# Performance work log

Measured on AMD Instinct MI355X. Metric: run time of the kernel, lower is better.

Reference implementation:

```python
import jax, jax.numpy as jnp
import numpy as np

N = 50000      # nodes
E = 800000     # directed edges
D = 128        # input_dim == hidden_dim
EL = 100000    # edges scored by decoder


def setup_inputs() -> dict:
    key = jax.random.key(0)
    ks = jax.random.split(key, 8)
    s = 1.0 / np.sqrt(D)  # glorot-ish scale
    return {
        "node_feature": jax.random.normal(ks[0], (N, D), jnp.float32),
        "W1": jax.random.normal(ks[1], (D, D), jnp.float32) * s,
        "b1": jnp.zeros((D,), jnp.float32),
        "W2": jax.random.normal(ks[2], (D, D), jnp.float32) * s,
        "b2": jnp.zeros((D,), jnp.float32),
        "W3": jax.random.normal(ks[3], (D, D), jnp.float32) * s,
        "b3": jnp.zeros((D,), jnp.float32),
        "edge_index": jax.random.randint(ks[4], (2, E), 0, N, dtype=jnp.int32),
        "edge_label_index": jax.random.randint(ks[5], (2, EL), 0, N, dtype=jnp.int32),
    }


def _gcn_conv(x, W, b, src, dst, norm, n):
    # x' = D^{-1/2} (A + I) D^{-1/2} (x W) + b   (PyG GCNConv semantics)
    h = x @ W                                   # [N, D]
    msg = h[src] * norm[:, None]                # gather + scale, [E+N, D]
    out = jax.ops.segment_sum(msg, dst, num_segments=n)  # scatter-add
    return out + b


def reference(node_feature, W1, b1, W2, b2, W3, b3, edge_index, edge_label_index):
    n = node_feature.shape[0]
    loop = jnp.arange(n, dtype=edge_index.dtype)
    src = jnp.concatenate([edge_index[0], loop])  # self-loops appended
    dst = jnp.concatenate([edge_index[1], loop])
    # symmetric normalization: deg over destinations (incl. self-loops)
    deg = jax.ops.segment_sum(jnp.ones_like(dst, dtype=node_feature.dtype), dst, num_segments=n)
    dinv = jax.lax.rsqrt(jnp.maximum(deg, 1.0))
    norm = dinv[src] * dinv[dst]                 # [E+N]

    x = jax.nn.relu(_gcn_conv(node_feature, W1, b1, src, dst, norm, n))
    x = jax.nn.relu(_gcn_conv(x, W2, b2, src, dst, norm, n))
    x = _gcn_conv(x, W3, b3, src, dst, norm, n)

    # dot-product edge decoder
    u = x[edge_label_index[0]]
    v = x[edge_label_index[1]]
    return jnp.sum(u * v, axis=-1)               # [EL] logits
```

## Files before the change

### kernel.cpp

```cpp
#include <hip/hip_runtime.h>
#include <hip/hip_bf16.h>
#include <hip/hip_fp16.h>

typedef _Float16 v8h __attribute__((ext_vector_type(8)));
typedef _Float16 v4h __attribute__((ext_vector_type(4)));
typedef float v4f __attribute__((ext_vector_type(4)));

__global__ __launch_bounds__(256) void wswz(const float* __restrict__ W1,
                                            const float* __restrict__ W2,
                                            const float* __restrict__ W3,
                                            __half* __restrict__ wfrag) {
    int o = blockIdx.x * 256 + threadIdx.x;
    int w = o >> 14, r = o & 16383;
    const float* Ws = (w >= 3) ? W3 : ((w == 2) ? W2 : W1);
    float v = Ws[r];
    __half h;
    if (w == 1) {
        __half hv = __float2half_rn(v);
        h = __float2half_rn(v - __half2float(hv));
    } else {
        h = __float2half_rn(v);
    }
    int k = r >> 7, ncol = r & 127;
    int c = ncol >> 4, nl = ncol & 15;
    int s = k >> 5, quad = (k >> 3) & 3, j = k & 7;
    int di = ((c * 4 + s) * 64 + quad * 16 + nl) * 8 + j;
    wfrag[(size_t)w * 16384 + di] = h;
}

__global__ __launch_bounds__(256) void deg_rank(const int* __restrict__ dst,
                                                int* __restrict__ cnt,
                                                int* __restrict__ rank, int E) {
    int base = blockIdx.x * 1024 + threadIdx.x * 4;
    if (base + 3 < E) {
        int4 d = *(const int4*)&dst[base];
        int r0 = atomicAdd(&cnt[d.x], 1);
        int r1 = atomicAdd(&cnt[d.y], 1);
        int r2 = atomicAdd(&cnt[d.z], 1);
        int r3 = atomicAdd(&cnt[d.w], 1);
        *(int4*)&rank[base] = make_int4(r0, r1, r2, r3);
    } else {
        for (int e = base; e < E; ++e) rank[e] = atomicAdd(&cnt[dst[e]], 1);
    }
}

__global__ __launch_bounds__(256) void gemm1(const float* __restrict__ X,
                                             const __half* __restrict__ wfrag,
                                             __half* __restrict__ H, int Nrows) {
    int tid = threadIdx.x;
    int rowbase = blockIdx.x * 64;
    int l = tid & 63;
    int wid = tid >> 6;
    int rb = wid * 16;
    int quad = l >> 4;
    int nn = l & 15;
    int gr = rowbase + rb + nn;
    v8h ah[4], al[4];
    if (gr < Nrows) {
        const float* Xr = &X[(size_t)gr * 128 + quad * 8];
#pragma unroll
        for (int k = 0; k < 4; ++k) {
            float4 f0 = *(const float4*)&Xr[k * 32];
            float4 f1 = *(const float4*)&Xr[k * 32 + 4];
            float ff[8] = {f0.x, f0.y, f0.z, f0.w, f1.x, f1.y, f1.z, f1.w};
            v8h h, lo;
#pragma unroll
            for (int m = 0; m < 8; ++m) {
                _Float16 hv = (_Float16)ff[m];
                h[m] = hv;
                lo[m] = (_Float16)(ff[m] - (float)hv);
            }
            ah[k] = h;
            al[k] = lo;
        }
    } else {
#pragma unroll
        for (int k = 0; k < 4; ++k) {
            v8h z;
#pragma unroll
            for (int m = 0; m < 8; ++m) z[m] = (_Float16)0.f;
            ah[k] = z;
            al[k] = z;
        }
    }
    const v8h* Wh = (const v8h*)wfrag;
    const v8h* Wl = (const v8h*)(wfrag + 16384);
    v4f acc[8] = {};
    v8h bh0 = Wh[0 * 64 + l];
    v8h bh1 = Wh[1 * 64 + l];
    v8h bh2 = Wh[2 * 64 + l];
    v8h bh3 = Wh[3 * 64 + l];
#pragma unroll
    for (int c = 0; c < 8; ++c) {
        v8h bl0 = Wl[(c * 4 + 0) * 64 + l];
        v8h bl1 = Wl[(c * 4 + 1) * 64 + l];
        v8h bl2 = Wl[(c * 4 + 2) * 64 + l];
        v8h bl3 = Wl[(c * 4 + 3) * 64 + l];
        acc[c] = __builtin_amdgcn_mfma_f32_16x16x32_f16(ah[0], bh0, acc[c], 0, 0, 0);
        acc[c] = __builtin_amdgcn_mfma_f32_16x16x32_f16(ah[1], bh1, acc[c], 0, 0, 0);
        acc[c] = __builtin_amdgcn_mfma_f32_16x16x32_f16(ah[2], bh2, acc[c], 0, 0, 0);
        acc[c] = __builtin_amdgcn_mfma_f32_16x16x32_f16(ah[3], bh3, acc[c], 0, 0, 0);
        acc[c] = __builtin_amdgcn_mfma_f32_16x16x32_f16(al[0], bh0, acc[c], 0, 0, 0);
        acc[c] = __builtin_amdgcn_mfma_f32_16x16x32_f16(al[1], bh1, acc[c], 0, 0, 0);
        acc[c] = __builtin_amdgcn_mfma_f32_16x16x32_f16(al[2], bh2, acc[c], 0, 0, 0);
        acc[c] = __builtin_amdgcn_mfma_f32_16x16x32_f16(al[3], bh3, acc[c], 0, 0, 0);
        v8h nh0, nh1, nh2, nh3;
        if (c < 7) {
            nh0 = Wh[((c + 1) * 4 + 0) * 64 + l];
            nh1 = Wh[((c + 1) * 4 + 1) * 64 + l];
            nh2 = Wh[((c + 1) * 4 + 2) * 64 + l];
            nh3 = Wh[((c + 1) * 4 + 3) * 64 + l];
        }
        acc[c] = __builtin_amdgcn_mfma_f32_16x16x32_f16(ah[0], bl0, acc[c], 0, 0, 0);
        acc[c] = __builtin_amdgcn_mfma_f32_16x16x32_f16(ah[1], bl1, acc[c], 0, 0, 0);
        acc[c] = __builtin_amdgcn_mfma_f32_16x16x32_f16(ah[2], bl2, acc[c], 0, 0, 0);
        acc[c] = __builtin_amdgcn_mfma_f32_16x16x32_f16(ah[3], bl3, acc[c], 0, 0, 0);
        if (c < 7) { bh0 = nh0; bh1 = nh1; bh2 = nh2; bh3 = nh3; }
    }
#pragma unroll
    for (int reg = 0; reg < 4; ++reg) {
        int grr = rowbase + rb + quad * 4 + reg;
        if (grr < Nrows) {
#pragma unroll
            for (int c = 0; c < 8; ++c)
                H[(size_t)grr * 128 + c * 16 + nn] = __float2half_rn(acc[c][reg]);
        }
    }
}

__global__ __launch_bounds__(256) void agg_gemm(const __half* __restrict__ Xs,
                                                const float* __restrict__ dinv,
                                                const int* __restrict__ rowptr,
                                                const int* __restrict__ col,
                                                const __half* __restrict__ wfrag,
                                                const float* __restrict__ bias,
                                                __half* __restrict__ Out,
                                                int n, int finalLayer) {
    __shared__ __align__(16) _Float16 y[64][136];
    int tid = threadIdx.x;
    int rowbase = blockIdx.x * 64;
    {
        int sub = tid >> 4;
        int t = (tid & 15) * 8;
        for (int g = 0; g < 4; ++g) {
            int rr = g * 16 + sub;
            int node = rowbase + rr;
            float a[8] = {};
            if (node < n) {
                int beg = rowptr[node], end = rowptr[node + 1];
                int k = beg;
                for (; k + 8 <= end; k += 8) {
                    int s0 = col[k], s1 = col[k + 1], s2 = col[k + 2], s3 = col[k + 3];
                    int s4 = col[k + 4], s5 = col[k + 5], s6 = col[k + 6], s7 = col[k + 7];
                    uint4 r0 = *(const uint4*)&Xs[(size_t)s0 * 128 + t];
                    uint4 r1 = *(const uint4*)&Xs[(size_t)s1 * 128 + t];
                    uint4 r2 = *(const uint4*)&Xs[(size_t)s2 * 128 + t];
                    uint4 r3 = *(const uint4*)&Xs[(size_t)s3 * 128 + t];
                    uint4 r4 = *(const uint4*)&Xs[(size_t)s4 * 128 + t];
                    uint4 r5 = *(const uint4*)&Xs[(size_t)s5 * 128 + t];
                    uint4 r6 = *(const uint4*)&Xs[(size_t)s6 * 128 + t];
                    uint4 r7 = *(const uint4*)&Xs[(size_t)s7 * 128 + t];
                    const __half2* h0 = (const __half2*)&r0;
                    const __half2* h1 = (const __half2*)&r1;
                    const __half2* h2 = (const __half2*)&r2;
                    const __half2* h3 = (const __half2*)&r3;
                    const __half2* h4 = (const __half2*)&r4;
                    const __half2* h5 = (const __half2*)&r5;
                    const __half2* h6 = (const __half2*)&r6;
                    const __half2* h7 = (const __half2*)&r7;
#pragma unroll
                    for (int m = 0; m < 4; ++m) {
                        float2 f0 = __half22float2(h0[m]);
                        float2 f1 = __half22float2(h1[m]);
                        float2 f2 = __half22float2(h2[m]);
                        float2 f3 = __half22float2(h3[m]);
                        float2 f4 = __half22float2(h4[m]);
                        float2 f5 = __half22float2(h5[m]);
                        float2 f6 = __half22float2(h6[m]);
                        float2 f7 = __half22float2(h7[m]);
                        a[2 * m]     += ((f0.x + f1.x) + (f2.x + f3.x)) + ((f4.x + f5.x) + (f6.x + f7.x));
                        a[2 * m + 1] += ((f0.y + f1.y) + (f2.y + f3.y)) + ((f4.y + f5.y) + (f6.y + f7.y));
                    }
                }
                for (; k + 4 <= end; k += 4) {
                    int s0 = col[k], s1 = col[k + 1], s2 = col[k + 2], s3 = col[k + 3];
                    uint4 r0 = *(const uint4*)&Xs[(size_t)s0 * 128 + t];
                    uint4 r1 = *(const uint4*)&Xs[(size_t)s1 * 128 + t];
                    uint4 r2 = *(const uint4*)&Xs[(size_t)s2 * 128 + t];
                    uint4 r3 = *(const uint4*)&Xs[(size_t)s3 * 128 + t];
                    const __half2* h0 = (const __half2*)&r0;
                    const __half2* h1 = (const __half2*)&r1;
                    const __half2* h2 = (const __half2*)&r2;
                    const __half2* h3 = (const __half2*)&r3;
#pragma unroll
                    for (int m = 0; m < 4; ++m) {
                        float2 f0 = __half22float2(h0[m]);
                        float2 f1 = __half22float2(h1[m]);
                        float2 f2 = __half22float2(h2[m]);
                        float2 f3 = __half22float2(h3[m]);
                        a[2 * m]     += (f0.x + f1.x) + (f2.x + f3.x);
                        a[2 * m + 1] += (f0.y + f1.y) + (f2.y + f3.y);
                    }
                }
                for (; k < end; ++k) {
                    uint4 r0 = *(const uint4*)&Xs[(size_t)col[k] * 128 + t];
                    const __half2* h0 = (const __half2*)&r0;
#pragma unroll
                    for (int m = 0; m < 4; ++m) {
                        float2 f0 = __half22float2(h0[m]);
                        a[2 * m] += f0.x;
                        a[2 * m + 1] += f0.y;
                    }
                }
                float dn = dinv[node];
#pragma unroll
                for (int m = 0; m < 8; ++m) a[m] *= dn;
            }
            v8h yv;
#pragma unroll
            for (int m = 0; m < 8; ++m) yv[m] = (_Float16)a[m];
            *(v8h*)&y[rr][t] = yv;
        }
    }
    __syncthreads();
    int l = tid & 63;
    int wid = tid >> 6;
    int rb = wid * 16;
    int quad = l >> 4;
    int nn = l & 15;
    v8h a0 = *(const v8h*)&y[rb + nn][0 * 32 + quad * 8];
    v8h a1 = *(const v8h*)&y[rb + nn][1 * 32 + quad * 8];
    v8h a2 = *(const v8h*)&y[rb + nn][2 * 32 + quad * 8];
    v8h a3 = *(const v8h*)&y[rb + nn][3 * 32 + quad * 8];
    const v8h* Wf = (const v8h*)wfrag;
    v4f acc[8] = {};
#pragma unroll
    for (int c = 0; c < 8; ++c) {
        v8h b0 = Wf[(c * 4 + 0) * 64 + l];
        v8h b1 = Wf[(c * 4 + 1) * 64 + l];
        v8h b2 = Wf[(c * 4 + 2) * 64 + l];
        v8h b3 = Wf[(c * 4 + 3) * 64 + l];
        acc[c] = __builtin_amdgcn_mfma_f32_16x16x32_f16(a0, b0, acc[c], 0, 0, 0);
        acc[c] = __builtin_amdgcn_mfma_f32_16x16x32_f16(a1, b1, acc[c], 0, 0, 0);
        acc[c] = __builtin_amdgcn_mfma_f32_16x16x32_f16(a2, b2, acc[c], 0, 0, 0);
        acc[c] = __builtin_amdgcn_mfma_f32_16x16x32_f16(a3, b3, acc[c], 0, 0, 0);
    }
#pragma unroll
    for (int reg = 0; reg < 4; ++reg) {
        int gr = rowbase + rb + quad * 4 + reg;
        if (gr < n) {
            float dn = dinv[gr];
#pragma unroll
            for (int c = 0; c < 8; ++c) {
                float z = acc[c][reg] + bias[c * 16 + nn];
                if (!finalLayer) z = fmaxf(z, 0.f) * dn;
                Out[(size_t)gr * 128 + c * 16 + nn] = __float2half_rn(z);
            }
        }
    }
}

__global__ void scanA(const int* __restrict__ cnt, int* __restrict__ tmp,
                      int* __restrict__ bsum, int n) {
    __shared__ int s[256];
    int i = blockIdx.x * 256 + threadIdx.x;
    int v = (i < n) ? (cnt[i] + 1) : 0;
    s[threadIdx.x] = v;
    __syncthreads();
    for (int off = 1; off < 256; off <<= 1) {
        int x = (threadIdx.x >= off) ? s[threadIdx.x - off] : 0;
        __syncthreads();
        s[threadIdx.x] += x;
        __syncthreads();
    }
    if (i < n) tmp[i] = s[threadIdx.x];
    if (threadIdx.x == 255) bsum[blockIdx.x] = s[255];
}

__global__ void scanB(const int* __restrict__ tmp, const int* __restrict__ bsum,
                      const int* __restrict__ cnt, int* __restrict__ rowptr,
                      float* __restrict__ dinv, int* __restrict__ col, int n, int nb) {
    __shared__ int p[256];
    int t = threadIdx.x;
    p[t] = (t < nb) ? bsum[t] : 0;
    __syncthreads();
    for (int off = 1; off < 256; off <<= 1) {
        int x = (t >= off) ? p[t - off] : 0;
        __syncthreads();
        p[t] += x;
        __syncthreads();
    }
    int prefix = (blockIdx.x == 0) ? 0 : p[blockIdx.x - 1];
    int i = blockIdx.x * 256 + t;
    if (i < n) {
        int inc = tmp[i] + prefix;
        rowptr[i + 1] = inc;
        int c1 = cnt[i] + 1;
        dinv[i] = rsqrtf((float)c1);
        col[inc - c1] = i;
        if (i == 0) rowptr[0] = 0;
    }
}

__global__ __launch_bounds__(256) void fill4(const int* __restrict__ src,
                                             const int* __restrict__ dst,
                                             const int* __restrict__ rank,
                                             const int* __restrict__ rowptr,
                                             int* __restrict__ col, int E) {
    int base = blockIdx.x * 1024 + threadIdx.x * 4;
    if (base + 3 < E) {
        int d0 = dst[base], d1 = dst[base + 1], d2 = dst[base + 2], d3 = dst[base + 3];
        int s0 = src[base], s1 = src[base + 1], s2 = src[base + 2], s3 = src[base + 3];
        int r0 = rank[base], r1 = rank[base + 1], r2 = rank[base + 2], r3 = rank[base + 3];
        col[rowptr[d0] + 1 + r0] = s0;
        col[rowptr[d1] + 1 + r1] = s1;
        col[rowptr[d2] + 1 + r2] = s2;
        col[rowptr[d3] + 1 + r3] = s3;
    } else {
        for (int e = base; e < E; ++e)
            col[rowptr[dst[e]] + 1 + rank[e]] = src[e];
    }
}

__global__ __launch_bounds__(256) void agg_h(const __half* __restrict__ H,
                                             const float* __restrict__ dinv,
                                             const int* __restrict__ rowptr,
                                             const int* __restrict__ col,
                                             const float* __restrict__ bias,
                                             __half* __restrict__ out, int n) {
    int node = blockIdx.x * 16 + (threadIdx.x >> 4);
    int t = (threadIdx.x & 15) * 8;
    if (node >= n) return;
    int beg = rowptr[node], end = rowptr[node + 1];
    float a[8] = {};
    int k = beg;
    for (; k + 8 <= end; k += 8) {
        int s0 = col[k], s1 = col[k + 1], s2 = col[k + 2], s3 = col[k + 3];
        int s4 = col[k + 4], s5 = col[k + 5], s6 = col[k + 6], s7 = col[k + 7];
        float w0 = dinv[s0], w1 = dinv[s1], w2 = dinv[s2], w3 = dinv[s3];
        float w4 = dinv[s4], w5 = dinv[s5], w6 = dinv[s6], w7 = dinv[s7];
        uint4 r0 = *(const uint4*)&H[(size_t)s0 * 128 + t];
        uint4 r1 = *(const uint4*)&H[(size_t)s1 * 128 + t];
        uint4 r2 = *(const uint4*)&H[(size_t)s2 * 128 + t];
        uint4 r3 = *(const uint4*)&H[(size_t)s3 * 128 + t];
        uint4 r4 = *(const uint4*)&H[(size_t)s4 * 128 + t];
        uint4 r5 = *(const uint4*)&H[(size_t)s5 * 128 + t];
        uint4 r6 = *(const uint4*)&H[(size_t)s6 * 128 + t];
        uint4 r7 = *(const uint4*)&H[(size_t)s7 * 128 + t];
        const __half2* h0 = (const __half2*)&r0;
        const __half2* h1 = (const __half2*)&r1;
        const __half2* h2 = (const __half2*)&r2;
        const __half2* h3 = (const __half2*)&r3;
        const __half2* h4 = (const __half2*)&r4;
        const __half2* h5 = (const __half2*)&r5;
        const __half2* h6 = (const __half2*)&r6;
        const __half2* h7 = (const __half2*)&r7;
#pragma unroll
        for (int m = 0; m < 4; ++m) {
            float2 f0 = __half22float2(h0[m]);
            float2 f1 = __half22float2(h1[m]);
            float2 f2 = __half22float2(h2[m]);
            float2 f3 = __half22float2(h3[m]);
            float2 f4 = __half22float2(h4[m]);
            float2 f5 = __half22float2(h5[m]);
            float2 f6 = __half22float2(h6[m]);
            float2 f7 = __half22float2(h7[m]);
            a[2 * m]     += (f0.x * w0 + f1.x * w1 + f2.x * w2 + f3.x * w3)
                          + (f4.x * w4 + f5.x * w5 + f6.x * w6 + f7.x * w7);
            a[2 * m + 1] += (f0.y * w0 + f1.y * w1 + f2.y * w2 + f3.y * w3)
                          + (f4.y * w4 + f5.y * w5 + f6.y * w6 + f7.y * w7);
        }
    }
    for (; k + 4 <= end; k += 4) {
        int s0 = col[k], s1 = col[k + 1], s2 = col[k + 2], s3 = col[k + 3];
        float w0 = dinv[s0], w1 = dinv[s1], w2 = dinv[s2], w3 = dinv[s3];
        uint4 r0 = *(const uint4*)&H[(size_t)s0 * 128 + t];
        uint4 r1 = *(const uint4*)&H[(size_t)s1 * 128 + t];
        uint4 r2 = *(const uint4*)&H[(size_t)s2 * 128 + t];
        uint4 r3 = *(const uint4*)&H[(size_t)s3 * 128 + t];
        const __half2* h0 = (const __half2*)&r0;
        const __half2* h1 = (const __half2*)&r1;
        const __half2* h2 = (const __half2*)&r2;
        const __half2* h3 = (const __half2*)&r3;
#pragma unroll
        for (int m = 0; m < 4; ++m) {
            float2 f0 = __half22float2(h0[m]);
            float2 f1 = __half22float2(h1[m]);
            float2 f2 = __half22float2(h2[m]);
            float2 f3 = __half22float2(h3[m]);
            a[2 * m]     += f0.x * w0 + f1.x * w1 + f2.x * w2 + f3.x * w3;
            a[2 * m + 1] += f0.y * w0 + f1.y * w1 + f2.y * w2 + f3.y * w3;
        }
    }
    for (; k < end; ++k) {
        int s0 = col[k];
        float w0 = dinv[s0];
        uint4 r0 = *(const uint4*)&H[(size_t)s0 * 128 + t];
        const __half2* h0 = (const __half2*)&r0;
#pragma unroll
        for (int m = 0; m < 4; ++m) {
            float2 f0 = __half22float2(h0[m]);
            a[2 * m] += f0.x * w0;
            a[2 * m + 1] += f0.y * w0;
        }
    }
    float dn = dinv[node];
    float4 b0 = *(const float4*)&bias[t];
    float4 b1 = *(const float4*)&bias[t + 4];
    float r0 = fmaxf(a[0] * dn + b0.x, 0.f) * dn;
    float r1 = fmaxf(a[1] * dn + b0.y, 0.f) * dn;
    float r2 = fmaxf(a[2] * dn + b0.z, 0.f) * dn;
    float r3 = fmaxf(a[3] * dn + b0.w, 0.f) * dn;
    float r4 = fmaxf(a[4] * dn + b1.x, 0.f) * dn;
    float r5 = fmaxf(a[5] * dn + b1.y, 0.f) * dn;
    float r6 = fmaxf(a[6] * dn + b1.z, 0.f) * dn;
    float r7 = fmaxf(a[7] * dn + b1.w, 0.f) * dn;
    auto pk = [](float x, float y) { __half2 h = __floats2half2_rn(x, y); return *(unsigned int*)&h; };
    uint4 o = make_uint4(pk(r0, r1), pk(r2, r3), pk(r4, r5), pk(r6, r7));
    *(uint4*)&out[(size_t)node * 128 + t] = o;
}

__global__ __launch_bounds__(256) void decoder_h(const __half* __restrict__ X,
                                                 const int* __restrict__ eli,
                                                 float* __restrict__ out, int EL) {
    int e = blockIdx.x * 16 + (threadIdx.x >> 4);
    int lane = threadIdx.x & 15;
    if (e >= EL) return;
    int u = eli[e], v = eli[EL + e];
    uint4 ra = *(const uint4*)&X[(size_t)u * 128 + lane * 8];
    uint4 rb = *(const uint4*)&X[(size_t)v * 128 + lane * 8];
    const __half2* ha = (const __half2*)&ra;
    const __half2* hb = (const __half2*)&rb;
    float d = 0.f;
#pragma unroll
    for (int j = 0; j < 4; ++j) {
        float2 fa = __half22float2(ha[j]);
        float2 fb = __half22float2(hb[j]);
        d += fa.x * fb.x + fa.y * fb.y;
    }
#pragma unroll
    for (int off = 8; off > 0; off >>= 1) d += __shfl_xor(d, off);
    if (lane == 0) out[e] = d;
}

extern "C" void kernel_launch(void* const* d_in, const int* in_sizes, int n_in,
                              void* d_out, int out_size, void* d_ws, size_t ws_size,
                              hipStream_t stream) {
    const float* x0 = (const float*)d_in[0];
    const float* W1 = (const float*)d_in[1];
    const float* b1 = (const float*)d_in[2];
    const float* W2 = (const float*)d_in[3];
    const float* b2 = (const float*)d_in[4];
    const float* W3 = (const float*)d_in[5];
    const float* b3 = (const float*)d_in[6];
    const int* ei   = (const int*)d_in[7];
    const int* eli  = (const int*)d_in[8];
    float* out = (float*)d_out;

    const int D = 128;
    const int N  = in_sizes[0] / D;
    const int E  = in_sizes[7] / 2;
    const int EL = in_sizes[8] / 2;

    const int* src = ei;
    const int* dst = ei + E;

    char* ws = (char*)d_ws;
    size_t off = 0;
    auto alloc = [&](size_t bytes) -> void* {
        off = (off + 255) & ~(size_t)255;
        void* p = ws + off;
        off += bytes;
        return p;
    };
    int*    cnt    = (int*)alloc((size_t)N * sizeof(int));
    int*    tmp    = (int*)alloc((size_t)N * sizeof(int));
    int*    bsum   = (int*)alloc(256 * sizeof(int));
    int*    rowptr = (int*)alloc((size_t)(N + 1) * sizeof(int));
    float*  dinv   = (float*)alloc((size_t)N * sizeof(float));
    int*    rank   = (int*)alloc((size_t)E * sizeof(int));
    int*    col    = (int*)alloc((size_t)(E + N) * sizeof(int));
    __half* wfrag  = (__half*)alloc((size_t)4 * 16384 * sizeof(__half));
    __half* hbuf   = (__half*)alloc((size_t)N * D * sizeof(__half));
    __half* xbuf   = (__half*)alloc((size_t)N * D * sizeof(__half));
    (void)ws_size;

    hipMemsetAsync(cnt, 0, (size_t)N * sizeof(int), stream);

    int nbN = (N + 255) / 256;
    int nbE4 = (E + 1023) / 1024;
    int gemmGrid = (N + 63) / 64;
    int fusedGrid = (N + 63) / 64;
    int aggGrid  = (N + 15) / 16;

    wswz<<<256, 256, 0, stream>>>(W1, W2, W3, wfrag);

    deg_rank<<<nbE4, 256, 0, stream>>>(dst, cnt, rank, E);
    gemm1<<<gemmGrid, 256, 0, stream>>>(x0, wfrag, hbuf, N);

    scanA<<<nbN, 256, 0, stream>>>(cnt, tmp, bsum, N);
    scanB<<<nbN, 256, 0, stream>>>(tmp, bsum, cnt, rowptr, dinv, col, N, nbN);
    fill4<<<nbE4, 256, 0, stream>>>(src, dst, rank, rowptr, col, E);

    agg_h<<<aggGrid, 256, 0, stream>>>(hbuf, dinv, rowptr, col, b1, xbuf, N);
    agg_gemm<<<fusedGrid, 256, 0, stream>>>(xbuf, dinv, rowptr, col, wfrag + 2 * 16384, b2, hbuf, N, 0);
    agg_gemm<<<fusedGrid, 256, 0, stream>>>(hbuf, dinv, rowptr, col, wfrag + 3 * 16384, b3, xbuf, N, 1);

    decoder_h<<<(EL + 15) / 16, 256, 0, stream>>>(xbuf, eli, out, EL);
}
```

Before: 275.1 us.

## Split fused aggregation+GEMM into separate kernels and merge degree counting into gemm1

The fused agg_gemm kernel is split into agg_plain, which gathers per node with 16 nodes per 256-thread block and writes an fp16 intermediate buffer, and gemm_post, which runs the MFMA GEMM directly from global memory. The intent is better load balance and occupancy for the irregular gather, since it no longer shares a block with LDS staging and a barrier. The cost is an extra N×128 fp16 write and read per layer and two more launches. Separately, the degree/rank atomics are folded into the first GEMM launch as extra blocks, each handling 8 edges per thread, which removes one launch and lets that work run alongside the GEMM.

Result: no change. 278.2 us (+1.1%).

```diff
diff --git a/kernel.cpp b/kernel.cpp
--- a/kernel.cpp
+++ b/kernel.cpp
@@ -28,27 +28,35 @@
     wfrag[(size_t)w * 16384 + di] = h;
 }
 
-__global__ __launch_bounds__(256) void deg_rank(const int* __restrict__ dst,
-                                                int* __restrict__ cnt,
-                                                int* __restrict__ rank, int E) {
-    int base = blockIdx.x * 1024 + threadIdx.x * 4;
-    if (base + 3 < E) {
-        int4 d = *(const int4*)&dst[base];
-        int r0 = atomicAdd(&cnt[d.x], 1);
-        int r1 = atomicAdd(&cnt[d.y], 1);
-        int r2 = atomicAdd(&cnt[d.z], 1);
-        int r3 = atomicAdd(&cnt[d.w], 1);
-        *(int4*)&rank[base] = make_int4(r0, r1, r2, r3);
-    } else {
-        for (int e = base; e < E; ++e) rank[e] = atomicAdd(&cnt[dst[e]], 1);
-    }
-}
-
-__global__ __launch_bounds__(256) void gemm1(const float* __restrict__ X,
-                                             const __half* __restrict__ wfrag,
-                                             __half* __restrict__ H, int Nrows) {
+__global__ __launch_bounds__(256) void gemm1_deg(const float* __restrict__ X,
+                                                 const __half* __restrict__ wfrag,
+                                                 __half* __restrict__ H, int Nrows,
+                                                 int degBlocks,
+                                                 const int* __restrict__ dst,
+                                                 int* __restrict__ cnt,
+                                                 int* __restrict__ rank, int E) {
     int tid = threadIdx.x;
-    int rowbase = blockIdx.x * 64;
+    if (blockIdx.x < degBlocks) {
+        int base = blockIdx.x * 2048 + tid * 8;
+        if (base + 7 < E) {
+            int4 d0 = *(const int4*)&dst[base];
+            int4 d1 = *(const int4*)&dst[base + 4];
+            int r0 = atomicAdd(&cnt[d0.x], 1);
+            int r1 = atomicAdd(&cnt[d0.y], 1);
+            int r2 = atomicAdd(&cnt[d0.z], 1);
+            int r3 = atomicAdd(&cnt[d0.w], 1);
+            int r4 = atomicAdd(&cnt[d1.x], 1);
+            int r5 = atomicAdd(&cnt[d1.y], 1);
+            int r6 = atomicAdd(&cnt[d1.z], 1);
+            int r7 = atomicAdd(&cnt[d1.w], 1);
+            *(int4*)&rank[base]     = make_int4(r0, r1, r2, r3);
+            *(int4*)&rank[base + 4] = make_int4(r4, r5, r6, r7);
+        } else {
+            for (int e = base; e < E; ++e) rank[e] = atomicAdd(&cnt[dst[e]], 1);
+        }
+        return;
+    }
+    int rowbase = (blockIdx.x - degBlocks) * 64;
     int l = tid & 63;
     int wid = tid >> 6;
     int rb = wid * 16;
@@ -128,110 +136,114 @@
     }
 }
 
-__global__ __launch_bounds__(256) void agg_gemm(const __half* __restrict__ Xs,
-                                                const float* __restrict__ dinv,
-                                                const int* __restrict__ rowptr,
-                                                const int* __restrict__ col,
-                                                const __half* __restrict__ wfrag,
-                                                const float* __restrict__ bias,
-                                                __half* __restrict__ Out,
-                                                int n, int finalLayer) {
-    __shared__ __align__(16) _Float16 y[64][136];
+__global__ __launch_bounds__(256) void agg_plain(const __half* __restrict__ Xs,
+                                                 const float* __restrict__ dinv,
+                                                 const int* __restrict__ rowptr,
+                                                 const int* __restrict__ col,
+                                                 __half* __restrict__ Y, int n) {
+    int node = blockIdx.x * 16 + (threadIdx.x >> 4);
+    int t = (threadIdx.x & 15) * 8;
+    if (node >= n) return;
+    int beg = rowptr[node], end = rowptr[node + 1];
+    float a[8] = {};
+    int k = beg;
+    for (; k + 8 <= end; k += 8) {
+        int s0 = col[k], s1 = col[k + 1], s2 = col[k + 2], s3 = col[k + 3];
+        int s4 = col[k + 4], s5 = col[k + 5], s6 = col[k + 6], s7 = col[k + 7];
+        uint4 r0 = *(const uint4*)&Xs[(size_t)s0 * 128 + t];
+        uint4 r1 = *(const uint4*)&Xs[(size_t)s1 * 128 + t];
+        uint4 r2 = *(const uint4*)&Xs[(size_t)s2 * 128 + t];
+        uint4 r3 = *(const uint4*)&Xs[(size_t)s3 * 128 + t];
+        uint4 r4 = *(const uint4*)&Xs[(size_t)s4 * 128 + t];
+        uint4 r5 = *(const uint4*)&Xs[(size_t)s5 * 128 + t];
+        uint4 r6 = *(const uint4*)&Xs[(size_t)s6 * 128 + t];
+        uint4 r7 = *(const uint4*)&Xs[(size_t)s7 * 128 + t];
+        const __half2* h0 = (const __half2*)&r0;
+        const __half2* h1 = (const __half2*)&r1;
+        const __half2* h2 = (const __half2*)&r2;
+        const __half2* h3 = (const __half2*)&r3;
+        const __half2* h4 = (const __half2*)&r4;
+        const __half2* h5 = (const __half2*)&r5;
+        const __half2* h6 = (const __half2*)&r6;
+        const __half2* h7 = (const __half2*)&r7;
+#pragma unroll
+        for (int m = 0; m < 4; ++m) {
+            float2 f0 = __half22float2(h0[m]);
+            float2 f1 = __half22float2(h1[m]);
+            float2 f2 = __half22float2(h2[m]);
+            float2 f3 = __half22float2(h3[m]);
+            float2 f4 = __half22float2(h4[m]);
+            float2 f5 = __half22float2(h5[m]);
+            float2 f6 = __half22float2(h6[m]);
+            float2 f7 = __half22float2(h7[m]);
+            a[2 * m]     += ((f0.x + f1.x) + (f2.x + f3.x)) + ((f4.x + f5.x) + (f6.x + f7.x));
+            a[2 * m + 1] += ((f0.y + f1.y) + (f2.y + f3.y)) + ((f4.y + f5.y) + (f6.y + f7.y));
+        }
+    }
+    for (; k + 4 <= end; k += 4) {
+        int s0 = col[k], s1 = col[k + 1], s2 = col[k + 2], s3 = col[k + 3];
+        uint4 r0 = *(const uint4*)&Xs[(size_t)s0 * 128 + t];
+        uint4 r1 = *(const uint4*)&Xs[(size_t)s1 * 128 + t];
+        uint4 r2 = *(const uint4*)&Xs[(size_t)s2 * 128 + t];
+        uint4 r3 = *(const uint4*)&Xs[(size_t)s3 * 128 + t];
+        const __half2* h0 = (const __half2*)&r0;
+        const __half2* h1 = (const __half2*)&r1;
+        const __half2* h2 = (const __half2*)&r2;
+        const __half2* h3 = (const __half2*)&r3;
+#pragma unroll
+        for (int m = 0; m < 4; ++m) {
+            float2 f0 = __half22float2(h0[m]);
+            float2 f1 = __half22float2(h1[m]);
+            float2 f2 = __half22float2(h2[m]);
+            float2 f3 = __half22float2(h3[m]);
+            a[2 * m]     += (f0.x + f1.x) + (f2.x + f3.x);
+            a[2 * m + 1] += (f0.y + f1.y) + (f2.y + f3.y);
+        }
+    }
+    for (; k < end; ++k) {
+        uint4 r0 = *(const uint4*)&Xs[(size_t)col[k] * 128 + t];
+        const __half2* h0 = (const __half2*)&r0;
+#pragma unroll
+        for (int m = 0; m < 4; ++m) {
+            float2 f0 = __half22float2(h0[m]);
+            a[2 * m] += f0.x;
+            a[2 * m + 1] += f0.y;
+        }
+    }
+    float dn = dinv[node];
+    auto pk = [](float x, float y) { __half2 h = __floats2half2_rn(x, y); return *(unsigned int*)&h; };
+    uint4 o = make_uint4(pk(a[0] * dn, a[1] * dn), pk(a[2] * dn, a[3] * dn),
+                         pk(a[4] * dn, a[5] * dn), pk(a[6] * dn, a[7] * dn));
+    *(uint4*)&Y[(size_t)node * 128 + t] = o;
+}
+
+__global__ __launch_bounds__(256) void gemm_post(const __half* __restrict__ Y,
+                                                 const float* __restrict__ dinv,
+                                                 const __half* __restrict__ wfrag,
+                                                 const float* __restrict__ bias,
+                                                 __half* __restrict__ Out,
+                                                 int n, int finalLayer) {
     int tid = threadIdx.x;
     int rowbase = blockIdx.x * 64;
-    {
-        int sub = tid >> 4;
-        int t = (tid & 15) * 8;
-        for (int g = 0; g < 4; ++g) {
-            int rr = g * 16 + sub;
-            int node = rowbase + rr;
-            float a[8] = {};
-            if (node < n) {
-                int beg = rowptr[node], end = rowptr[node + 1];
-                int k = beg;
-                for (; k + 8 <= end; k += 8) {
-                    int s0 = col[k], s1 = col[k + 1], s2 = col[k + 2], s3 = col[k + 3];
-                    int s4 = col[k + 4], s5 = col[k + 5], s6 = col[k + 6], s7 = col[k + 7];
-                    uint4 r0 = *(const uint4*)&Xs[(size_t)s0 * 128 + t];
-                    uint4 r1 = *(const uint4*)&Xs[(size_t)s1 * 128 + t];
-                    uint4 r2 = *(const uint4*)&Xs[(size_t)s2 * 128 + t];
-                    uint4 r3 = *(const uint4*)&Xs[(size_t)s3 * 128 + t];
-                    uint4 r4 = *(const uint4*)&Xs[(size_t)s4 * 128 + t];
-                    uint4 r5 = *(const uint4*)&Xs[(size_t)s5 * 128 + t];
-                    uint4 r6 = *(const uint4*)&Xs[(size_t)s6 * 128 + t];
-                    uint4 r7 = *(const uint4*)&Xs[(size_t)s7 * 128 + t];
-                    const __half2* h0 = (const __half2*)&r0;
-                    const __half2* h1 = (const __half2*)&r1;
-                    const __half2* h2 = (const __half2*)&r2;
-                    const __half2* h3 = (const __half2*)&r3;
-                    const __half2* h4 = (const __half2*)&r4;
-                    const __half2* h5 = (const __half2*)&r5;
-                    const __half2* h6 = (const __half2*)&r6;
-                    const __half2* h7 = (const __half2*)&r7;
-#pragma unroll
-                    for (int m = 0; m < 4; ++m) {
-                        float2 f0 = __half22float2(h0[m]);
-                        float2 f1 = __half22float2(h1[m]);
-                        float2 f2 = __half22float2(h2[m]);
-                        float2 f3 = __half22float2(h3[m]);
-                        float2 f4 = __half22float2(h4[m]);
-                        float2 f5 = __half22float2(h5[m]);
-                        float2 f6 = __half22float2(h6[m]);
-                        float2 f7 = __half22float2(h7[m]);
-                        a[2 * m]     += ((f0.x + f1.x) + (f2.x + f3.x)) + ((f4.x + f5.x) + (f6.x + f7.x));
-                        a[2 * m + 1] += ((f0.y + f1.y) + (f2.y + f3.y)) + ((f4.y + f5.y) + (f6.y + f7.y));
-                    }
-                }
-                for (; k + 4 <= end; k += 4) {
-                    int s0 = col[k], s1 = col[k + 1], s2 = col[k + 2], s3 = col[k + 3];
-                    uint4 r0 = *(const uint4*)&Xs[(size_t)s0 * 128 + t];
-                    uint4 r1 = *(const uint4*)&Xs[(size_t)s1 * 128 + t];
-                    uint4 r2 = *(const uint4*)&Xs[(size_t)s2 * 128 + t];
-                    uint4 r3 = *(const uint4*)&Xs[(size_t)s3 * 128 + t];
-                    const __half2* h0 = (const __half2*)&r0;
-                    const __half2* h1 = (const __half2*)&r1;
-                    const __half2* h2 = (const __half2*)&r2;
-                    const __half2* h3 = (const __half2*)&r3;
-#pragma unroll
-                    for (int m = 0; m < 4; ++m) {
-                        float2 f0 = __half22float2(h0[m]);
-                        float2 f1 = __half22float2(h1[m]);
-                        float2 f2 = __half22float2(h2[m]);
-                        float2 f3 = __half22float2(h3[m]);
-                        a[2 * m]     += (f0.x + f1.x) + (f2.x + f3.x);
-                        a[2 * m + 1] += (f0.y + f1.y) + (f2.y + f3.y);
-                    }
-                }
-                for (; k < end; ++k) {
-                    uint4 r0 = *(const uint4*)&Xs[(size_t)col[k] * 128 + t];
-                    const __half2* h0 = (const __half2*)&r0;
-#pragma unroll
-                    for (int m = 0; m < 4; ++m) {
-                        float2 f0 = __half22float2(h0[m]);
-                        a[2 * m] += f0.x;
-                        a[2 * m + 1] += f0.y;
-                    }
-                }
-                float dn = dinv[node];
-#pragma unroll
-                for (int m = 0; m < 8; ++m) a[m] *= dn;
-            }
-            v8h yv;
-#pragma unroll
-            for (int m = 0; m < 8; ++m) yv[m] = (_Float16)a[m];
-            *(v8h*)&y[rr][t] = yv;
-        }
-    }
-    __syncthreads();
     int l = tid & 63;
     int wid = tid >> 6;
     int rb = wid * 16;
     int quad = l >> 4;
     int nn = l & 15;
-    v8h a0 = *(const v8h*)&y[rb + nn][0 * 32 + quad * 8];
-    v8h a1 = *(const v8h*)&y[rb + nn][1 * 32 + quad * 8];
-    v8h a2 = *(const v8h*)&y[rb + nn][2 * 32 + quad * 8];
-    v8h a3 = *(const v8h*)&y[rb + nn][3 * 32 + quad * 8];
+    int gr = rowbase + rb + nn;
+    v8h a0, a1, a2, a3;
+    if (gr < n) {
+        const __half* Yr = &Y[(size_t)gr * 128 + quad * 8];
+        a0 = *(const v8h*)&Yr[0];
+        a1 = *(const v8h*)&Yr[32];
+        a2 = *(const v8h*)&Yr[64];
+        a3 = *(const v8h*)&Yr[96];
+    } else {
+        v8h z;
+#pragma unroll
+        for (int m = 0; m < 8; ++m) z[m] = (_Float16)0.f;
+        a0 = z; a1 = z; a2 = z; a3 = z;
+    }
     const v8h* Wf = (const v8h*)wfrag;
     v4f acc[8] = {};
 #pragma unroll
@@ -247,14 +259,14 @@
     }
 #pragma unroll
     for (int reg = 0; reg < 4; ++reg) {
-        int gr = rowbase + rb + quad * 4 + reg;
-        if (gr < n) {
-            float dn = dinv[gr];
+        int grr = rowbase + rb + quad * 4 + reg;
+        if (grr < n) {
+            float dn = dinv[grr];
 #pragma unroll
             for (int c = 0; c < 8; ++c) {
                 float z = acc[c][reg] + bias[c * 16 + nn];
                 if (!finalLayer) z = fmaxf(z, 0.f) * dn;
-                Out[(size_t)gr * 128 + c * 16 + nn] = __float2half_rn(z);
+                Out[(size_t)grr * 128 + c * 16 + nn] = __float2half_rn(z);
             }
         }
     }
@@ -483,28 +495,33 @@
     __half* wfrag  = (__half*)alloc((size_t)4 * 16384 * sizeof(__half));
     __half* hbuf   = (__half*)alloc((size_t)N * D * sizeof(__half));
     __half* xbuf   = (__half*)alloc((size_t)N * D * sizeof(__half));
+    __half* ybuf   = (__half*)alloc((size_t)N * D * sizeof(__half));
     (void)ws_size;
 
     hipMemsetAsync(cnt, 0, (size_t)N * sizeof(int), stream);
 
     int nbN = (N + 255) / 256;
     int nbE4 = (E + 1023) / 1024;
+    int nbE8 = (E + 2047) / 2048;
     int gemmGrid = (N + 63) / 64;
-    int fusedGrid = (N + 63) / 64;
     int aggGrid  = (N + 15) / 16;
 
     wswz<<<256, 256, 0, stream>>>(W1, W2, W3, wfrag);
 
-    deg_rank<<<nbE4, 256, 0, stream>>>(dst, cnt, rank, E);
-    gemm1<<<gemmGrid, 256, 0, stream>>>(x0, wfrag, hbuf, N);
+    gemm1_deg<<<nbE8 + gemmGrid, 256, 0, stream>>>(x0, wfrag, hbuf, N,
+                                                   nbE8, dst, cnt, rank, E);
 
     scanA<<<nbN, 256, 0, stream>>>(cnt, tmp, bsum, N);
     scanB<<<nbN, 256, 0, stream>>>(tmp, bsum, cnt, rowptr, dinv, col, N, nbN);
     fill4<<<nbE4, 256, 0, stream>>>(src, dst, rank, rowptr, col, E);
 
     agg_h<<<aggGrid, 256, 0, stream>>>(hbuf, dinv, rowptr, col, b1, xbuf, N);
-    agg_gemm<<<fusedGrid, 256, 0, stream>>>(xbuf, dinv, rowptr, col, wfrag + 2 * 16384, b2, hbuf, N, 0);
-    agg_gemm<<<fusedGrid, 256, 0, stream>>>(hbuf, dinv, rowptr, col, wfrag + 3 * 16384, b3, xbuf, N, 1);
+
+    agg_plain<<<aggGrid, 256, 0, stream>>>(xbuf, dinv, rowptr, col, ybuf, N);
+    gemm_post<<<gemmGrid, 256, 0, stream>>>(ybuf, dinv, wfrag + 2 * 16384, b2, hbuf, N, 0);
+
+    agg_plain<<<aggGrid, 256, 0, stream>>>(hbuf, dinv, rowptr, col, ybuf, N);
+    gemm_post<<<gemmGrid, 256, 0, stream>>>(ybuf, dinv, wfrag + 3 * 16384, b3, xbuf, N, 1);
 
     decoder_h<<<(EL + 15) / 16, 256, 0, stream>>>(xbuf, eli, out, EL);
 }
```
